# Optimization experiments

Hardware: AMD Instinct MI355X
Metric: run time of the kernel (lower is better)

The kernel has to match this reference:

```python
import jax, jax.numpy as jnp
import numpy as np

N = 4096      # nodes (= attention seq_len)
D = 256       # dim_h
H = 4         # num_heads
HD = D // H   # head dim
E = 131072    # edges (avg degree 32)


def _ln(x, g, b, eps=1e-5):
    mu = jnp.mean(x, -1, keepdims=True)
    var = jnp.var(x, -1, keepdims=True)
    return (x - mu) * jax.lax.rsqrt(var + eps) * g + b


def setup_inputs() -> dict:
    key = jax.random.key(0)
    ks = jax.random.split(key, 10)
    s = 0.02
    nrm = lambda k, shape: jax.random.normal(k, shape, jnp.float32) * s
    return dict(
        x=jax.random.normal(ks[0], (N, D), jnp.float32),
        edge_index=jax.random.randint(ks[1], (2, E), 0, N, dtype=jnp.int32),
        W_gcn=nrm(ks[2], (D, D)), b_gcn=jnp.zeros((D,), jnp.float32),
        w_qkv=nrm(ks[3], (D, 3 * D)), b_qkv=jnp.zeros((3 * D,), jnp.float32),
        w_out=nrm(ks[4], (D, D)), b_out=jnp.zeros((D,), jnp.float32),
        g1l=jnp.ones((D,), jnp.float32), beta1l=jnp.zeros((D,), jnp.float32),
        g1a=jnp.ones((D,), jnp.float32), beta1a=jnp.zeros((D,), jnp.float32),
        W1=nrm(ks[5], (D, 2 * D)), bf1=jnp.zeros((2 * D,), jnp.float32),
        W2=nrm(ks[6], (2 * D, D)), bf2=jnp.zeros((D,), jnp.float32),
        g2=jnp.ones((D,), jnp.float32), beta2=jnp.zeros((D,), jnp.float32),
    )


def reference(x, edge_index, W_gcn, b_gcn, w_qkv, b_qkv, w_out, b_out,
              g1l, beta1l, g1a, beta1a, W1, bf1, W2, bf2, g2, beta2):
    n = x.shape[0]
    # --- GCNConv: sym-normalized aggregation with self loops ---
    loop = jnp.arange(n, dtype=edge_index.dtype)
    src = jnp.concatenate([edge_index[0], loop])
    dst = jnp.concatenate([edge_index[1], loop])
    deg = jax.ops.segment_sum(jnp.ones_like(src, x.dtype), dst, num_segments=n)
    dinv = jax.lax.rsqrt(deg)  # deg >= 1 thanks to self loops
    h = x @ W_gcn                                  # [N, D]
    msg = h[src] * (dinv[src] * dinv[dst])[:, None]  # gather + edge norm
    x_local = jax.ops.segment_sum(msg, dst, num_segments=n) + b_gcn
    x = _ln(x + x_local, g1l, beta1l)
    # --- Multi-head self-attention over all nodes (one sequence) ---
    qkv = x @ w_qkv + b_qkv
    q, k, v = jnp.split(qkv, 3, axis=-1)
    q = q.reshape(n, H, HD)
    k = k.reshape(n, H, HD)
    v = v.reshape(n, H, HD)
    scale = 1.0 / (HD ** 0.5)
    scores = jnp.einsum('nhd,mhd->hnm', q, k) * scale   # [H, N, N]
    attn = jax.nn.softmax(scores, axis=-1)
    x_attn = jnp.einsum('hnm,mhd->nhd', attn, v).reshape(n, D) @ w_out + b_out
    x = _ln(x + x_attn, g1a, beta1a)
    # --- FFN (D -> 2D -> D, ReLU) ---
    x_ffn = jax.nn.relu(x @ W1 + bf1) @ W2 + bf2
    return _ln(x + x_ffn, g2, beta2)
```

## Files before the change

### kernel.cpp

```cpp
#include <hip/hip_runtime.h>

typedef unsigned short u16;
typedef __bf16 bf16x8 __attribute__((ext_vector_type(8)));
typedef float f32x4 __attribute__((ext_vector_type(4)));

__device__ __forceinline__ u16 f2u(float f) {
    unsigned u = __builtin_bit_cast(unsigned, f);
    return (u16)((u + 0x7FFFu + ((u >> 16) & 1u)) >> 16);
}

__device__ __forceinline__ void glds16(const u16* g, u16* l) {
    __builtin_amdgcn_global_load_lds((const __attribute__((address_space(1))) unsigned int*)g,
                                     (__attribute__((address_space(3))) unsigned int*)l, 16, 0, 0);
}


__global__ __launch_bounds__(256) void prep_k(
    const float* __restrict__ w0, const float* __restrict__ w1, const float* __restrict__ w2,
    const float* __restrict__ w3, const float* __restrict__ w4, const float* __restrict__ x,
    u16* __restrict__ o0, u16* __restrict__ o1, u16* __restrict__ o2,
    u16* __restrict__ o3, u16* __restrict__ o4, u16* __restrict__ xo,
    int* __restrict__ cnt, int xblocks, int nn) {
    int b = blockIdx.x, t = threadIdx.x;
    if (b < 144) {
        const float* in; u16* out; int R, C, tb;
        if (b < 16)       { in = w0; out = o0; R = 256; C = 256; tb = b; }
        else if (b < 64)  { in = w1; out = o1; R = 256; C = 768; tb = b - 16; }
        else if (b < 80)  { in = w2; out = o2; R = 256; C = 256; tb = b - 64; }
        else if (b < 112) { in = w3; out = o3; R = 256; C = 512; tb = b - 80; }
        else              { in = w4; out = o4; R = 512; C = 256; tb = b - 112; }
        int tcols = C >> 6;
        int tr = tb / tcols, tc = tb - tr * tcols;
        __shared__ float T[64][65];
        int i0 = t >> 6, j = t & 63;
#pragma unroll
        for (int p = 0; p < 16; p++) {
            int r = p * 4 + i0;
            T[r][j] = in[(long)(tr * 64 + r) * C + tc * 64 + j];
        }
        __syncthreads();
#pragma unroll
        for (int p = 0; p < 16; p++) {
            int c = p * 4 + i0;
            out[(long)(tc * 64 + c) * R + tr * 64 + j] = f2u(T[j][c]);
        }
    } else if (b < 144 + xblocks) {
        long base = (long)(b - 144) * 4096;
#pragma unroll
        for (int p = 0; p < 4; p++) {
            long idx = base + p * 1024 + t * 4;
            float4 v = *(const float4*)&x[idx];
            unsigned lo = (unsigned)f2u(v.x) | ((unsigned)f2u(v.y) << 16);
            unsigned hi = (unsigned)f2u(v.z) | ((unsigned)f2u(v.w) << 16);
            *(uint2*)&xo[idx] = uint2{lo, hi};
        }
    } else {
        int i = (b - 144 - xblocks) * 256 + t;
        if (i < nn) cnt[i] = 0;
    }
}

__global__ void count_k(const int* __restrict__ ei, int E, int* __restrict__ cnt) {
    int e = blockIdx.x * 256 + threadIdx.x;
    if (e < E) atomicAdd(&cnt[ei[E + e]], 1);
}

__global__ __launch_bounds__(256) void scan_k(const int* __restrict__ cnt, int* __restrict__ offs,
                                              int* __restrict__ cur, float* __restrict__ dinv) {
    __shared__ int sums[256];
    int t = threadIdx.x;
    int base = t * 16;
    int loc[16]; int s = 0;
#pragma unroll
    for (int i = 0; i < 16; i++) { loc[i] = s; s += cnt[base + i]; }
    sums[t] = s;
    __syncthreads();
    for (int off = 1; off < 256; off <<= 1) {
        int v = (t >= off) ? sums[t - off] : 0;
        __syncthreads();
        sums[t] += v;
        __syncthreads();
    }
    int ex = (t == 0) ? 0 : sums[t - 1];
#pragma unroll
    for (int i = 0; i < 16; i++) {
        int o = ex + loc[i];
        offs[base + i] = o; cur[base + i] = o;
        dinv[base + i] = rsqrtf((float)(cnt[base + i] + 1));
    }
}

__global__ void scatter_k(const int* __restrict__ ei, int E, int* __restrict__ cur, int* __restrict__ srcs) {
    int e = blockIdx.x * 256 + threadIdx.x;
    if (e < E) {
        int s = ei[e], d = ei[E + e];
        int p = atomicAdd(&cur[d], 1);
        srcs[p] = s;
    }
}


__device__ __forceinline__ void block_ln_stats(float v, float& mu, float& rstd) {
    float s1 = v, s2 = v * v;
#pragma unroll
    for (int m = 1; m < 64; m <<= 1) { s1 += __shfl_xor(s1, m, 64); s2 += __shfl_xor(s2, m, 64); }
    __shared__ float r1[4], r2[4];
    int lane = threadIdx.x & 63, w = threadIdx.x >> 6;
    if (lane == 0) { r1[w] = s1; r2[w] = s2; }
    __syncthreads();
    s1 = r1[0] + r1[1] + r1[2] + r1[3];
    s2 = r2[0] + r2[1] + r2[2] + r2[3];
    mu = s1 * (1.0f / 256.0f);
    float var = s2 * (1.0f / 256.0f) - mu * mu;
    rstd = rsqrtf(var + 1e-5f);
}

__global__ __launch_bounds__(256) void ln_k(const float* __restrict__ a, const float* __restrict__ b,
                                            const float* __restrict__ g, const float* __restrict__ be,
                                            float* __restrict__ out, u16* __restrict__ outbf) {
    int n = blockIdx.x, d = threadIdx.x;
    long i = (long)n * 256 + d;
    float v = a[i] + b[i];
    float mu, rs;
    block_ln_stats(v, mu, rs);
    float y = (v - mu) * rs * g[d] + be[d];
    out[i] = y;
    if (outbf) outbf[i] = f2u(y);
}


__global__ __launch_bounds__(256) void gcn_agg_ln_k(
    const float* __restrict__ h, const float* __restrict__ x,
    const int* __restrict__ srcs, const int* __restrict__ offs, const int* __restrict__ cnt,
    const float* __restrict__ dinv, const float* __restrict__ bg,
    const float* __restrict__ g, const float* __restrict__ be,
    float* __restrict__ x1, u16* __restrict__ x1bf) {
    int n = blockIdx.x, d = threadIdx.x;
    int c = cnt[n], st = offs[n];
    float dn = dinv[n];
    float agg = h[(long)n * 256 + d] * dn;
    int e = 0;
    for (; e + 4 <= c; e += 4) {
        int s0 = srcs[st + e], s1 = srcs[st + e + 1], s2 = srcs[st + e + 2], s3 = srcs[st + e + 3];
        float a0 = h[(long)s0 * 256 + d] * dinv[s0];
        float a1 = h[(long)s1 * 256 + d] * dinv[s1];
        float a2 = h[(long)s2 * 256 + d] * dinv[s2];
        float a3 = h[(long)s3 * 256 + d] * dinv[s3];
        agg += (a0 + a1) + (a2 + a3);
    }
    for (; e < c; e++) {
        int s = srcs[st + e];
        agg += h[(long)s * 256 + d] * dinv[s];
    }
    float v = x[(long)n * 256 + d] + dn * agg + bg[d];
    float mu, rs;
    block_ln_stats(v, mu, rs);
    float y = (v - mu) * rs * g[d] + be[d];
    x1[(long)n * 256 + d] = y;
    x1bf[(long)n * 256 + d] = f2u(y);
}


template <int EPI>
__global__ __launch_bounds__(256) void gemm_k(
    const u16* __restrict__ A, const u16* __restrict__ Bt,
    const float* __restrict__ bias, void* __restrict__ outp,
    int M, int N, int K) {
    __shared__ __align__(16) u16 AB[2][2][2048];
    int tid = threadIdx.x;
    int lane = tid & 63, w = tid >> 6;
    int l15 = lane & 15, quad = lane >> 4;
    int m0 = blockIdx.x * 64, n0 = blockIdx.y * 64;
    int wm = (w >> 1) * 32, wn = (w & 1) * 32;
    f32x4 acc[2][2];
#pragma unroll
    for (int i = 0; i < 2; i++)
#pragma unroll
        for (int j = 0; j < 2; j++) acc[i][j] = f32x4{0.f, 0.f, 0.f, 0.f};

    int sj = tid >> 2;
    int sq = (tid & 3) ^ ((sj >> 1) & 3);
    const u16* ap = A + (long)(m0 + sj) * K + sq * 8;
    const u16* bp = Bt + (long)(n0 + sj) * K + sq * 8;
    u16* la0 = &AB[0][0][tid * 8]; u16* lb0 = &AB[0][1][tid * 8];
    u16* la1 = &AB[1][0][tid * 8]; u16* lb1 = &AB[1][1][tid * 8];

    int ma0 = wm + l15, ma1 = wm + 16 + l15;
    int na0 = wn + l15, na1 = wn + 16 + l15;
    int offA0 = ma0 * 32 + ((quad ^ ((ma0 >> 1) & 3)) << 3);
    int offA1 = ma1 * 32 + ((quad ^ ((ma1 >> 1) & 3)) << 3);
    int offB0 = na0 * 32 + ((quad ^ ((na0 >> 1) & 3)) << 3);
    int offB1 = na1 * 32 + ((quad ^ ((na1 >> 1) & 3)) << 3);

    glds16(ap, la0); glds16(bp, lb0);
    ap += 32; bp += 32;

    int nit = K >> 5;
    for (int it = 0; it < nit; it++) {
        __syncthreads();
        if (it + 1 < nit) {
            if (it & 1) { glds16(ap, la0); glds16(bp, lb0); }
            else        { glds16(ap, la1); glds16(bp, lb1); }
            ap += 32; bp += 32;
        }
        const u16* As = &AB[it & 1][0][0];
        const u16* Bs = &AB[it & 1][1][0];
        bf16x8 af0 = *(const bf16x8*)&As[offA0];
        bf16x8 af1 = *(const bf16x8*)&As[offA1];
        bf16x8 bf0 = *(const bf16x8*)&Bs[offB0];
        bf16x8 bf1 = *(const bf16x8*)&Bs[offB1];
        acc[0][0] = __builtin_amdgcn_mfma_f32_16x16x32_bf16(af0, bf0, acc[0][0], 0, 0, 0);
        acc[0][1] = __builtin_amdgcn_mfma_f32_16x16x32_bf16(af0, bf1, acc[0][1], 0, 0, 0);
        acc[1][0] = __builtin_amdgcn_mfma_f32_16x16x32_bf16(af1, bf0, acc[1][0], 0, 0, 0);
        acc[1][1] = __builtin_amdgcn_mfma_f32_16x16x32_bf16(af1, bf1, acc[1][1], 0, 0, 0);
    }

#pragma unroll
    for (int nf = 0; nf < 2; nf++) {
        int col = n0 + wn + nf * 16 + l15;
        float bv = bias ? bias[col] : 0.0f;
#pragma unroll
        for (int mf = 0; mf < 2; mf++) {
#pragma unroll
            for (int r = 0; r < 4; r++) {
                int row = m0 + wm + mf * 16 + quad * 4 + r;
                float v = acc[mf][nf][r] + bv;
                if (EPI == 0) {
                    ((float*)outp)[(long)row * N + col] = v;
                } else if (EPI == 1) {
                    u16* q = (u16*)outp;
                    u16* kk = q + (long)M * 256;
                    u16* vt = kk + (long)M * 256;
                    if (col < 256) {
                        q[(((col >> 6) * (long)M) + row) * 64 + (col & 63)] = f2u(v * 0.180336884f);
                    } else if (col < 512) {
                        int c = col - 256;
                        kk[(((c >> 6) * (long)M) + row) * 64 + (c & 63)] = f2u(v);
                    } else {
                        int c = col - 512;
                        vt[((c >> 6) * 64 + (c & 63)) * (long)M + row] = f2u(v);
                    }
                } else {
                    ((u16*)outp)[(long)row * N + col] = f2u(v > 0.f ? v : 0.f);
                }
            }
        }
    }
}


__global__ __launch_bounds__(256) void attn_k(const u16* __restrict__ qg, const u16* __restrict__ kg,
                                              const u16* __restrict__ vtg, float* __restrict__ po,
                                              float* __restrict__ pl, int N, int S) {
    int tid = threadIdx.x;
    int w = tid >> 6, lane = tid & 63, l15 = lane & 15, quad = lane >> 4;
    int lid = blockIdx.x + 64 * blockIdx.y + 256 * blockIdx.z;
    int hs = lid & 15;
    int hh = hs & 3, sp = hs >> 2, qb = lid >> 4;
    int q0 = qb * 64 + w * 16;
    int kbeg = sp * (N / S);
    int nit = (N / S) / 64;
    const u16* qh = qg + (long)hh * N * 64;
    const u16* kh = kg + (long)hh * N * 64;
    const u16* vh = vtg + (long)hh * 64 * N;

    __shared__ __align__(16) u16 KV[2][2][4096];
    __shared__ __align__(16) u16 P[4][1024];
    u16* Pw = &P[w][0];

    int s0 = tid, j0 = s0 >> 3, c0s = ((s0 & 7) ^ (j0 & 7)) * 8;
    int s1 = tid + 256, j1 = s1 >> 3, c1s = ((s1 & 7) ^ (j1 & 7)) * 8;
    const u16* kp0 = kh + (long)(kbeg + j0) * 64 + c0s;
    const u16* kp1 = kh + (long)(kbeg + j1) * 64 + c1s;
    const u16* vp0 = vh + (long)j0 * N + kbeg + c0s;
    const u16* vp1 = vh + (long)j1 * N + kbeg + c1s;
    u16* lk0[2] = {&KV[0][0][s0 * 8], &KV[1][0][s0 * 8]};
    u16* lk1[2] = {&KV[0][0][s1 * 8], &KV[1][0][s1 * 8]};
    u16* lv0[2] = {&KV[0][1][s0 * 8], &KV[1][1][s0 * 8]};
    u16* lv1[2] = {&KV[0][1][s1 * 8], &KV[1][1][s1 * 8]};

    int lo3 = l15 & 7, hi = l15 >> 3;
    int c0 = (quad ^ lo3) * 8;
    int c1 = c0 ^ 32;

    bf16x8 aq0 = *(const bf16x8*)(qh + (long)(q0 + l15) * 64 + quad * 8);
    bf16x8 aq1 = *(const bf16x8*)(qh + (long)(q0 + l15) * 64 + 32 + quad * 8);
    f32x4 o[4];
#pragma unroll
    for (int dn = 0; dn < 4; dn++) o[dn] = f32x4{0.f, 0.f, 0.f, 0.f};
    float ls[4] = {0.f, 0.f, 0.f, 0.f};

    glds16(kp0, lk0[0]); glds16(kp1, lk1[0]);
    glds16(vp0, lv0[0]); glds16(vp1, lv1[0]);
    kp0 += 4096; kp1 += 4096; vp0 += 64; vp1 += 64;

    for (int it = 0; it < nit; it++) {
        __syncthreads();
        if (it + 1 < nit) {
            int nb = (it + 1) & 1;
            glds16(kp0, lk0[nb]); glds16(kp1, lk1[nb]);
            glds16(vp0, lv0[nb]); glds16(vp1, lv1[nb]);
            kp0 += 4096; kp1 += 4096; vp0 += 64; vp1 += 64;
        }
        const u16* Kc = &KV[it & 1][0][0];
        const u16* Vc = &KV[it & 1][1][0];
#pragma unroll
        for (int nt = 0; nt < 4; nt++) {
            const u16* Kr = Kc + (nt * 16 + l15) * 64;
            bf16x8 b0 = *(const bf16x8*)(Kr + c0);
            bf16x8 b1 = *(const bf16x8*)(Kr + c1);
            f32x4 s = f32x4{0.f, 0.f, 0.f, 0.f};
            s = __builtin_amdgcn_mfma_f32_16x16x32_bf16(aq0, b0, s, 0, 0, 0);
            s = __builtin_amdgcn_mfma_f32_16x16x32_bf16(aq1, b1, s, 0, 0, 0);
#pragma unroll
            for (int r = 0; r < 4; r++) {
                float e = exp2f(s[r]);
                ls[r] += e;
                int row = quad * 4 + r;
                Pw[row * 64 + ((((nt << 1) | hi) ^ (row & 7)) << 3) + lo3] = f2u(e);
            }
        }
        bf16x8 pa0 = *(const bf16x8*)&Pw[l15 * 64 + c0];
        bf16x8 pa1 = *(const bf16x8*)&Pw[l15 * 64 + c1];
#pragma unroll
        for (int dn = 0; dn < 4; dn++) {
            const u16* Vr = Vc + (dn * 16 + l15) * 64;
            bf16x8 v0 = *(const bf16x8*)(Vr + c0);
            bf16x8 v1 = *(const bf16x8*)(Vr + c1);
            o[dn] = __builtin_amdgcn_mfma_f32_16x16x32_bf16(pa0, v0, o[dn], 0, 0, 0);
            o[dn] = __builtin_amdgcn_mfma_f32_16x16x32_bf16(pa1, v1, o[dn], 0, 0, 0);
        }
    }

#pragma unroll
    for (int r = 0; r < 4; r++) {
        float v = ls[r];
        v += __shfl_xor(v, 1, 64);
        v += __shfl_xor(v, 2, 64);
        v += __shfl_xor(v, 4, 64);
        v += __shfl_xor(v, 8, 64);
        ls[r] = v;
    }
    long pbase = ((long)(sp * 4 + hh)) * N;
#pragma unroll
    for (int dn = 0; dn < 4; dn++)
#pragma unroll
        for (int r = 0; r < 4; r++) {
            int row = q0 + quad * 4 + r;
            po[(pbase + row) * 64 + dn * 16 + l15] = o[dn][r];
        }
    if (l15 == 0) {
#pragma unroll
        for (int r = 0; r < 4; r++) pl[pbase + q0 + quad * 4 + r] = ls[r];
    }
}

__global__ __launch_bounds__(256) void attn_comb_k(const float* __restrict__ po, const float* __restrict__ pl,
                                                   u16* __restrict__ xo, int N, int S) {
    int n = blockIdx.x, c = threadIdx.x;
    int hh = c >> 6, d = c & 63;
    float osum = 0.f, lsum = 0.f;
    for (int s = 0; s < S; s++) {
        osum += po[(((long)(s * 4 + hh)) * N + n) * 64 + d];
        lsum += pl[((long)(s * 4 + hh)) * N + n];
    }
    xo[(long)n * 256 + c] = f2u(osum / lsum);
}


extern "C" void kernel_launch(void* const* d_in, const int* in_sizes, int n_in,
                              void* d_out, int out_size, void* d_ws, size_t ws_size,
                              hipStream_t stream) {
    const float* x    = (const float*)d_in[0];
    const int*   ei   = (const int*)d_in[1];
    const float* Wg   = (const float*)d_in[2];
    const float* bg   = (const float*)d_in[3];
    const float* Wqkv = (const float*)d_in[4];
    const float* bqkv = (const float*)d_in[5];
    const float* Wo   = (const float*)d_in[6];
    const float* bo   = (const float*)d_in[7];
    const float* g1l  = (const float*)d_in[8];
    const float* b1l  = (const float*)d_in[9];
    const float* g1a  = (const float*)d_in[10];
    const float* b1a  = (const float*)d_in[11];
    const float* W1   = (const float*)d_in[12];
    const float* bf1  = (const float*)d_in[13];
    const float* W2   = (const float*)d_in[14];
    const float* bf2  = (const float*)d_in[15];
    const float* g2   = (const float*)d_in[16];
    const float* b2   = (const float*)d_in[17];
    float* out = (float*)d_out;

    int N = in_sizes[0] / 256;
    int E = in_sizes[1] / 2;
    const int S = 4;

    char* p = (char*)d_ws;
    auto alloc = [&](size_t bytes) { void* r = (void*)p; p += (bytes + 255) & ~(size_t)255; return r; };
    u16*   wg_t   = (u16*)alloc((size_t)256 * 256 * 2);
    u16*   wqkv_t = (u16*)alloc((size_t)256 * 768 * 2);
    u16*   wo_t   = (u16*)alloc((size_t)256 * 256 * 2);
    u16*   w1_t   = (u16*)alloc((size_t)512 * 256 * 2);
    u16*   w2_t   = (u16*)alloc((size_t)256 * 512 * 2);
    u16*   xbf    = (u16*)alloc((size_t)N * 256 * 2);
    float* h      = (float*)alloc((size_t)N * 256 * 4);
    int*   cnt    = (int*)alloc((size_t)N * 4);
    int*   offs   = (int*)alloc((size_t)N * 4);
    int*   cur    = (int*)alloc((size_t)N * 4);
    float* dinv   = (float*)alloc((size_t)N * 4);
    int*   srcs   = (int*)alloc((size_t)E * 4);
    float* x1     = (float*)alloc((size_t)N * 256 * 4);
    u16*   x1bf   = (u16*)alloc((size_t)N * 256 * 2);
    u16*   qkv    = (u16*)alloc((size_t)3 * N * 256 * 2);
    u16*   xattn  = (u16*)alloc((size_t)N * 256 * 2);
    float* attno  = (float*)alloc((size_t)N * 256 * 4);
    float* x2     = (float*)alloc((size_t)N * 256 * 4);
    u16*   x2bf   = (u16*)alloc((size_t)N * 256 * 2);
    u16*   ffn1   = (u16*)alloc((size_t)N * 512 * 2);
    float* ffno   = (float*)alloc((size_t)N * 256 * 4);
    float* po     = (float*)alloc((size_t)S * 4 * N * 64 * 4);
    float* pl     = (float*)alloc((size_t)S * 4 * N * 4);

    dim3 b256(256);

    int xblocks = (N * 256) / 4096;
    int cblocks = (N + 255) / 256;
    prep_k<<<144 + xblocks + cblocks, b256, 0, stream>>>(Wg, Wqkv, Wo, W1, W2, x,
                                                         wg_t, wqkv_t, wo_t, w1_t, w2_t, xbf,
                                                         cnt, xblocks, N);

    count_k<<<(E + 255) / 256, b256, 0, stream>>>(ei, E, cnt);
    scan_k<<<1, b256, 0, stream>>>(cnt, offs, cur, dinv);
    scatter_k<<<(E + 255) / 256, b256, 0, stream>>>(ei, E, cur, srcs);

    gemm_k<0><<<dim3(N / 64, 4), b256, 0, stream>>>(xbf, wg_t, nullptr, h, N, 256, 256);
    gcn_agg_ln_k<<<N, b256, 0, stream>>>(h, x, srcs, offs, cnt, dinv, bg, g1l, b1l, x1, x1bf);

    gemm_k<1><<<dim3(N / 64, 12), b256, 0, stream>>>(x1bf, wqkv_t, bqkv, qkv, N, 768, 256);
    attn_k<<<dim3(N / 64, 4, S), b256, 0, stream>>>(qkv, qkv + (size_t)N * 256, qkv + (size_t)2 * N * 256,
                                                    po, pl, N, S);
    attn_comb_k<<<N, b256, 0, stream>>>(po, pl, xattn, N, S);
    gemm_k<0><<<dim3(N / 64, 4), b256, 0, stream>>>(xattn, wo_t, bo, attno, N, 256, 256);
    ln_k<<<N, b256, 0, stream>>>(x1, attno, g1a, b1a, x2, x2bf);

    gemm_k<2><<<dim3(N / 64, 8), b256, 0, stream>>>(x2bf, w1_t, bf1, ffn1, N, 512, 256);
    gemm_k<0><<<dim3(N / 64, 4), b256, 0, stream>>>(ffn1, w2_t, bf2, ffno, N, 256, 512);
    ln_k<<<N, b256, 0, stream>>>(x2, ffno, g2, b2, out, nullptr);
}
```

Before: 220.0 us.

## Stage full K-slab in GEMM and transpose score MFMA in attention

The GEMM now loads a 64x256 K-slab of A and B into LDS at once with an XOR swizzle and runs 8 MFMA steps per barrier, replacing the per-32 double-buffered loop. This cuts barrier count but drops the overlap of loads with compute and raises LDS use per block. The attention kernel swaps the MFMA operands so each lane holds four consecutive key scores for one query. P is then packed to bf16 with perm and written as 8-byte stores, and the row-sum uses truncated bf16 values, reduced with two shuffles instead of four per row.

```diff
diff --git a/kernel.cpp b/kernel.cpp
--- a/kernel.cpp
+++ b/kernel.cpp
@@ -166,10 +166,11 @@
     const u16* __restrict__ A, const u16* __restrict__ Bt,
     const float* __restrict__ bias, void* __restrict__ outp,
     int M, int N, int K) {
-    __shared__ __align__(16) u16 AB[2][2][2048];
+    __shared__ __align__(16) u16 As[64 * 256];
+    __shared__ __align__(16) u16 Bs[64 * 256];
     int tid = threadIdx.x;
     int lane = tid & 63, w = tid >> 6;
-    int l15 = lane & 15, quad = lane >> 4;
+    int l15 = lane & 15, quad = lane >> 4, l7 = l15 & 7;
     int m0 = blockIdx.x * 64, n0 = blockIdx.y * 64;
     int wm = (w >> 1) * 32, wn = (w & 1) * 32;
     f32x4 acc[2][2];
@@ -178,41 +179,32 @@
 #pragma unroll
         for (int j = 0; j < 2; j++) acc[i][j] = f32x4{0.f, 0.f, 0.f, 0.f};
 
-    int sj = tid >> 2;
-    int sq = (tid & 3) ^ ((sj >> 1) & 3);
-    const u16* ap = A + (long)(m0 + sj) * K + sq * 8;
-    const u16* bp = Bt + (long)(n0 + sj) * K + sq * 8;
-    u16* la0 = &AB[0][0][tid * 8]; u16* lb0 = &AB[0][1][tid * 8];
-    u16* la1 = &AB[1][0][tid * 8]; u16* lb1 = &AB[1][1][tid * 8];
-
-    int ma0 = wm + l15, ma1 = wm + 16 + l15;
-    int na0 = wn + l15, na1 = wn + 16 + l15;
-    int offA0 = ma0 * 32 + ((quad ^ ((ma0 >> 1) & 3)) << 3);
-    int offA1 = ma1 * 32 + ((quad ^ ((ma1 >> 1) & 3)) << 3);
-    int offB0 = na0 * 32 + ((quad ^ ((na0 >> 1) & 3)) << 3);
-    int offB1 = na1 * 32 + ((quad ^ ((na1 >> 1) & 3)) << 3);
-
-    glds16(ap, la0); glds16(bp, lb0);
-    ap += 32; bp += 32;
-
-    int nit = K >> 5;
-    for (int it = 0; it < nit; it++) {
+    int rA0 = (wm + l15) * 256, rA1 = (wm + 16 + l15) * 256;
+    int rB0 = (wn + l15) * 256, rB1 = (wn + 16 + l15) * 256;
+
+    for (int kb = 0; kb < K; kb += 256) {
+        if (kb) __syncthreads();
+#pragma unroll
+        for (int i = 0; i < 8; i++) {
+            int s = i * 256 + tid;
+            int j = s >> 5, dch = s & 31;
+            int c = dch ^ (j & 7);
+            glds16(A + (long)(m0 + j) * K + kb + c * 8, &As[s * 8]);
+            glds16(Bt + (long)(n0 + j) * K + kb + c * 8, &Bs[s * 8]);
+        }
         __syncthreads();
-        if (it + 1 < nit) {
-            if (it & 1) { glds16(ap, la0); glds16(bp, lb0); }
-            else        { glds16(ap, la1); glds16(bp, lb1); }
-            ap += 32; bp += 32;
-        }
-        const u16* As = &AB[it & 1][0][0];
-        const u16* Bs = &AB[it & 1][1][0];
-        bf16x8 af0 = *(const bf16x8*)&As[offA0];
-        bf16x8 af1 = *(const bf16x8*)&As[offA1];
-        bf16x8 bf0 = *(const bf16x8*)&Bs[offB0];
-        bf16x8 bf1 = *(const bf16x8*)&Bs[offB1];
-        acc[0][0] = __builtin_amdgcn_mfma_f32_16x16x32_bf16(af0, bf0, acc[0][0], 0, 0, 0);
-        acc[0][1] = __builtin_amdgcn_mfma_f32_16x16x32_bf16(af0, bf1, acc[0][1], 0, 0, 0);
-        acc[1][0] = __builtin_amdgcn_mfma_f32_16x16x32_bf16(af1, bf0, acc[1][0], 0, 0, 0);
-        acc[1][1] = __builtin_amdgcn_mfma_f32_16x16x32_bf16(af1, bf1, acc[1][1], 0, 0, 0);
+#pragma unroll
+        for (int step = 0; step < 8; step++) {
+            int d8 = (((step << 2) + quad) ^ l7) << 3;
+            bf16x8 af0 = *(const bf16x8*)&As[rA0 + d8];
+            bf16x8 af1 = *(const bf16x8*)&As[rA1 + d8];
+            bf16x8 bf0 = *(const bf16x8*)&Bs[rB0 + d8];
+            bf16x8 bf1 = *(const bf16x8*)&Bs[rB1 + d8];
+            acc[0][0] = __builtin_amdgcn_mfma_f32_16x16x32_bf16(af0, bf0, acc[0][0], 0, 0, 0);
+            acc[0][1] = __builtin_amdgcn_mfma_f32_16x16x32_bf16(af0, bf1, acc[0][1], 0, 0, 0);
+            acc[1][0] = __builtin_amdgcn_mfma_f32_16x16x32_bf16(af1, bf0, acc[1][0], 0, 0, 0);
+            acc[1][1] = __builtin_amdgcn_mfma_f32_16x16x32_bf16(af1, bf1, acc[1][1], 0, 0, 0);
+        }
     }
 
 #pragma unroll
@@ -279,16 +271,19 @@
     u16* lv0[2] = {&KV[0][1][s0 * 8], &KV[1][1][s0 * 8]};
     u16* lv1[2] = {&KV[0][1][s1 * 8], &KV[1][1][s1 * 8]};
 
-    int lo3 = l15 & 7, hi = l15 >> 3;
+    int lo3 = l15 & 7;
     int c0 = (quad ^ lo3) * 8;
     int c1 = c0 ^ 32;
+    int ps = lo3 << 1;
+    int pw0 = l15 * 64 + (((quad << 1) ^ ps) << 2);
+    int pw1 = l15 * 64 + (((8 + (quad << 1)) ^ ps) << 2);
 
     bf16x8 aq0 = *(const bf16x8*)(qh + (long)(q0 + l15) * 64 + quad * 8);
     bf16x8 aq1 = *(const bf16x8*)(qh + (long)(q0 + l15) * 64 + 32 + quad * 8);
     f32x4 o[4];
 #pragma unroll
     for (int dn = 0; dn < 4; dn++) o[dn] = f32x4{0.f, 0.f, 0.f, 0.f};
-    float ls[4] = {0.f, 0.f, 0.f, 0.f};
+    float lsum = 0.f;
 
     glds16(kp0, lk0[0]); glds16(kp1, lk1[0]);
     glds16(vp0, lv0[0]); glds16(vp1, lv1[0]);
@@ -307,21 +302,26 @@
 #pragma unroll
         for (int nt = 0; nt < 4; nt++) {
             const u16* Kr = Kc + (nt * 16 + l15) * 64;
-            bf16x8 b0 = *(const bf16x8*)(Kr + c0);
-            bf16x8 b1 = *(const bf16x8*)(Kr + c1);
+            bf16x8 kf0 = *(const bf16x8*)(Kr + c0);
+            bf16x8 kf1 = *(const bf16x8*)(Kr + c1);
             f32x4 s = f32x4{0.f, 0.f, 0.f, 0.f};
-            s = __builtin_amdgcn_mfma_f32_16x16x32_bf16(aq0, b0, s, 0, 0, 0);
-            s = __builtin_amdgcn_mfma_f32_16x16x32_bf16(aq1, b1, s, 0, 0, 0);
-#pragma unroll
-            for (int r = 0; r < 4; r++) {
-                float e = exp2f(s[r]);
-                ls[r] += e;
-                int row = quad * 4 + r;
-                Pw[row * 64 + ((((nt << 1) | hi) ^ (row & 7)) << 3) + lo3] = f2u(e);
-            }
-        }
-        bf16x8 pa0 = *(const bf16x8*)&Pw[l15 * 64 + c0];
-        bf16x8 pa1 = *(const bf16x8*)&Pw[l15 * 64 + c1];
+            s = __builtin_amdgcn_mfma_f32_16x16x32_bf16(kf0, aq0, s, 0, 0, 0);
+            s = __builtin_amdgcn_mfma_f32_16x16x32_bf16(kf1, aq1, s, 0, 0, 0);
+            unsigned u0 = __builtin_bit_cast(unsigned, exp2f(s[0]));
+            unsigned u1 = __builtin_bit_cast(unsigned, exp2f(s[1]));
+            unsigned u2 = __builtin_bit_cast(unsigned, exp2f(s[2]));
+            unsigned u3 = __builtin_bit_cast(unsigned, exp2f(s[3]));
+            lsum += __builtin_bit_cast(float, u0 & 0xFFFF0000u);
+            lsum += __builtin_bit_cast(float, u1 & 0xFFFF0000u);
+            lsum += __builtin_bit_cast(float, u2 & 0xFFFF0000u);
+            lsum += __builtin_bit_cast(float, u3 & 0xFFFF0000u);
+            unsigned pk01 = __builtin_amdgcn_perm(u1, u0, 0x07060302u);
+            unsigned pk23 = __builtin_amdgcn_perm(u3, u2, 0x07060302u);
+            int pc = ((nt * 4 + quad) ^ ps) << 2;
+            *(uint2*)&Pw[l15 * 64 + pc] = uint2{pk01, pk23};
+        }
+        bf16x8 pa0 = *(const bf16x8*)&Pw[pw0];
+        bf16x8 pa1 = *(const bf16x8*)&Pw[pw1];
 #pragma unroll
         for (int dn = 0; dn < 4; dn++) {
             const u16* Vr = Vc + (dn * 16 + l15) * 64;
@@ -332,15 +332,9 @@
         }
     }
 
-#pragma unroll
-    for (int r = 0; r < 4; r++) {
-        float v = ls[r];
-        v += __shfl_xor(v, 1, 64);
-        v += __shfl_xor(v, 2, 64);
-        v += __shfl_xor(v, 4, 64);
-        v += __shfl_xor(v, 8, 64);
-        ls[r] = v;
-    }
+    lsum += __shfl_xor(lsum, 16, 64);
+    lsum += __shfl_xor(lsum, 32, 64);
+
     long pbase = ((long)(sp * 4 + hh)) * N;
 #pragma unroll
     for (int dn = 0; dn < 4; dn++)
@@ -349,10 +343,7 @@
             int row = q0 + quad * 4 + r;
             po[(pbase + row) * 64 + dn * 16 + l15] = o[dn][r];
         }
-    if (l15 == 0) {
-#pragma unroll
-        for (int r = 0; r < 4; r++) pl[pbase + q0 + quad * 4 + r] = ls[r];
-    }
+    if (quad == 0) pl[pbase + q0 + l15] = lsum;
 }
 
 __global__ __launch_bounds__(256) void attn_comb_k(const float* __restrict__ po, const float* __restrict__ pl,
```

New measurement: 213.1 us. 1.03x faster.
